# Kernel tuning notes

Measured on AMD Instinct MI355X. Metric: run time of the kernel, lower is better.

The kernel has to match this reference:

```python
import jax, jax.numpy as jnp
import numpy as np

B, S, HID = 2, 2048, 2048
NH, NKV, D = 32, 8, 64
G = NH // NKV  # kv groups


def rotate_half(x):
    x1, x2 = jnp.split(x, 2, axis=-1)
    return jnp.concatenate([-x2, x1], axis=-1)


def setup_inputs() -> dict:
    key = jax.random.key(0)
    ks = jax.random.split(key, 6)
    hidden_states = jax.random.normal(ks[0], (B, S, HID), dtype=jnp.float32)
    # rotary tables [S, D]
    inv_freq = 1.0 / (10000.0 ** (jnp.arange(0, D, 2, dtype=jnp.float32) / D))
    t = jnp.arange(S, dtype=jnp.float32)
    freqs = jnp.einsum('s,d->sd', t, inv_freq)
    emb = jnp.concatenate([freqs, freqs], axis=-1)
    cos, sin = jnp.cos(emb), jnp.sin(emb)
    # additive causal mask [B,1,S,S]
    causal = jnp.triu(jnp.full((S, S), -1e9, dtype=jnp.float32), k=1)
    attention_mask = jnp.broadcast_to(causal, (B, 1, S, S))
    sc = 0.02
    wq = jax.random.normal(ks[1], (HID, 2 * NH * D), dtype=jnp.float32) * sc
    wk = jax.random.normal(ks[2], (HID, NKV * D), dtype=jnp.float32) * sc
    wv = jax.random.normal(ks[3], (HID, NKV * D), dtype=jnp.float32) * sc
    wo = jax.random.normal(ks[4], (HID, HID), dtype=jnp.float32) * sc
    return {"hidden_states": hidden_states, "cos": cos, "sin": sin,
            "attention_mask": attention_mask, "wq": wq, "wk": wk, "wv": wv, "wo": wo}


def reference(hidden_states, cos, sin, attention_mask, wq, wk, wv, wo):
    b, s, _ = hidden_states.shape
    qg = hidden_states @ wq                      # [B,S,2*NH*D]
    q, gate = jnp.split(qg, 2, axis=-1)
    q = q.reshape(b, s, NH, D).transpose(0, 2, 1, 3)        # [B,NH,S,D]
    k = (hidden_states @ wk).reshape(b, s, NKV, D).transpose(0, 2, 1, 3)
    v = (hidden_states @ wv).reshape(b, s, NKV, D).transpose(0, 2, 1, 3)  # computed, unused (as in source)
    # RoPE (cos/sin broadcast over batch and heads)
    c = cos[None, None]; sn = sin[None, None]
    q = q * c + rotate_half(q) * sn
    k = k * c + rotate_half(k) * sn
    # GQA repeat_kv
    k = jnp.repeat(k, G, axis=1)                 # [B,NH,S,D]
    # no 1/sqrt(d) scaling in source
    attn = jnp.einsum('bhqd,bhkd->bhqk', q, k) + attention_mask
    w = jax.nn.softmax(attn.astype(jnp.float32), axis=-1).astype(q.dtype)
    # NOTE: source multiplies weights by key_states (not value_states) — reproduced faithfully
    out = jnp.einsum('bhqk,bhkd->bhqd', w, k)
    out = out.transpose(0, 2, 1, 3).reshape(b, s, HID)
    out = out * jax.nn.sigmoid(gate)
    return out @ wo
```

## Files before the change

kernel.cpp:

```cpp
#include <hip/hip_runtime.h>

typedef float f32x4 __attribute__((ext_vector_type(4)));
typedef short bf16x8 __attribute__((ext_vector_type(8)));

__device__ __forceinline__ float bf2f(unsigned short h) {
  return __uint_as_float(((unsigned int)h) << 16);
}
__device__ __forceinline__ unsigned short f2bf(float f) {
  unsigned int u = __float_as_uint(f);
  unsigned int r = u + 0x7fffu + ((u >> 16) & 1u);
  return (unsigned short)(r >> 16);
}
__device__ __forceinline__ float fast_exp2(float x) {
  return __builtin_amdgcn_exp2f(x);
}
__device__ __forceinline__ unsigned cvt_pk_bf16(float lo, float hi) {
  unsigned d;
  asm("v_cvt_pk_bf16_f32 %0, %1, %2" : "=v"(d) : "v"(lo), "v"(hi));
  return d;
}
__device__ __forceinline__ float max3f(float a, float b, float c) {
  float d;
  asm("v_max3_f32 %0, %1, %2, %3" : "=v"(d) : "v"(a), "v"(b), "v"(c));
  return d;
}

__device__ __forceinline__ void gload_lds16(const void* g, void* l) {
  __builtin_amdgcn_global_load_lds((const __attribute__((address_space(1))) void*)g,
                                   (__attribute__((address_space(3))) void*)l, 16, 0, 0);
}

__global__ void conv_bf16(const float* __restrict__ src, unsigned short* __restrict__ dst, int n4) {
  for (int i = blockIdx.x * blockDim.x + threadIdx.x; i < n4; i += gridDim.x * blockDim.x) {
    float4 v = ((const float4*)src)[i];
    ushort4 o;
    o.x = f2bf(v.x); o.y = f2bf(v.y); o.z = f2bf(v.z); o.w = f2bf(v.w);
    ((ushort4*)dst)[i] = o;
  }
}

__global__ void conv_cs(const float* __restrict__ cosT, const float* __restrict__ sinT,
                        unsigned* __restrict__ cs, int n) {
  int i = blockIdx.x * blockDim.x + threadIdx.x;
  if (i < n) cs[i] = cvt_pk_bf16(cosT[i], sinT[i]);
}

__global__ void tconv(const float* __restrict__ src, unsigned short* __restrict__ dst,
                      int C, int dstRowOff, int dstLD) {
  __shared__ float tile[32][33];
  int c0 = blockIdx.x * 32, r0 = blockIdx.y * 32;
  int tx = threadIdx.x, ty = threadIdx.y;
#pragma unroll
  for (int i = 0; i < 4; ++i)
    tile[ty + i * 8][tx] = src[(size_t)(r0 + ty + i * 8) * C + c0 + tx];
  __syncthreads();
#pragma unroll
  for (int i = 0; i < 4; ++i)
    dst[(size_t)(dstRowOff + c0 + ty + i * 8) * dstLD + r0 + tx] = f2bf(tile[tx][ty + i * 8]);
}

template <typename OutT>
__global__ __launch_bounds__(256) void gemm_bt(const unsigned short* __restrict__ A,
                                               const unsigned short* __restrict__ BT,
                                               OutT* __restrict__ C, int M, int N, int K) {
  __shared__ unsigned short As[128 * 64];
  __shared__ unsigned short Bs[128 * 64];
  const int tid = threadIdx.x;
  const int lane = tid & 63;
  const int wid = tid >> 6;
  const int g = lane >> 4, l15 = lane & 15;
  const int wr = wid >> 1, wc = wid & 1;
  const int bm = blockIdx.y, bn = blockIdx.x;
  const unsigned short* Ab = A + (size_t)bm * 128 * K;
  const unsigned short* Bb = BT + (size_t)bn * 128 * K;
  f32x4 acc[4][4] = {};
  int Rj[4], csj[4];
#pragma unroll
  for (int j = 0; j < 4; ++j) {
    int c = j * 256 + tid;
    Rj[j] = c >> 3;
    csj[j] = ((c & 7) ^ (Rj[j] & 7)) * 8;
  }
  for (int k0 = 0; k0 < K; k0 += 64) {
#pragma unroll
    for (int j = 0; j < 4; ++j) {
      gload_lds16(Ab + (size_t)Rj[j] * K + k0 + csj[j], &As[(j * 256 + (wid << 6)) * 8]);
      gload_lds16(Bb + (size_t)Rj[j] * K + k0 + csj[j], &Bs[(j * 256 + (wid << 6)) * 8]);
    }
    __syncthreads();
    bf16x8 af[4][2], bfr[4][2];
#pragma unroll
    for (int i = 0; i < 4; ++i)
#pragma unroll
      for (int kk = 0; kk < 2; ++kk) {
        int rowa = wr * 64 + i * 16 + l15;
        int cha = ((kk * 4 + g) ^ (rowa & 7)) * 8;
        af[i][kk] = *(const bf16x8*)&As[rowa * 64 + cha];
        int rowb = wc * 64 + i * 16 + l15;
        int chb = ((kk * 4 + g) ^ (rowb & 7)) * 8;
        bfr[i][kk] = *(const bf16x8*)&Bs[rowb * 64 + chb];
      }
    __builtin_amdgcn_s_setprio(1);
#pragma unroll
    for (int kk = 0; kk < 2; ++kk)
#pragma unroll
      for (int i = 0; i < 4; ++i)
#pragma unroll
        for (int j = 0; j < 4; ++j)
          acc[i][j] = __builtin_amdgcn_mfma_f32_16x16x32_bf16(af[i][kk], bfr[j][kk], acc[i][j], 0, 0, 0);
    __builtin_amdgcn_s_setprio(0);
    __syncthreads();
  }
  const int rbase = bm * 128 + wr * 64 + ((lane >> 4) << 2);
  const int cbase = bn * 128 + wc * 64 + l15;
#pragma unroll
  for (int i = 0; i < 4; ++i)
#pragma unroll
    for (int j = 0; j < 4; ++j)
#pragma unroll
      for (int r = 0; r < 4; ++r) {
        int row = rbase + i * 16 + r;
        int col = cbase + j * 16;
        if constexpr (sizeof(OutT) == 2)
          C[(size_t)row * N + col] = f2bf(acc[i][j][r]);
        else
          C[(size_t)row * N + col] = acc[i][j][r];
      }
}

__global__ __launch_bounds__(256) void gemm_qgk(const unsigned short* __restrict__ A,
                                                const unsigned short* __restrict__ BT,
                                                const unsigned* __restrict__ cs,
                                                unsigned short* __restrict__ qrope,
                                                unsigned short* __restrict__ gateb,
                                                unsigned short* __restrict__ krope) {
  const int K = 2048;
  __shared__ unsigned short As[128 * 64];
  __shared__ unsigned short Bs[128 * 64];
  const int tid = threadIdx.x;
  const int lane = tid & 63;
  const int wid = tid >> 6;
  const int g = lane >> 4, l15 = lane & 15;
  const int wr = wid >> 1, wc = wid & 1;
  const int bm = blockIdx.y, bn = blockIdx.x;
  const unsigned short* Ab = A + (size_t)bm * 128 * K;
  const unsigned short* Bb = BT + (size_t)bn * 128 * K;
  f32x4 acc[4][4] = {};
  int Rj[4], csj[4];
#pragma unroll
  for (int j = 0; j < 4; ++j) {
    int c = j * 256 + tid;
    Rj[j] = c >> 3;
    csj[j] = ((c & 7) ^ (Rj[j] & 7)) * 8;
  }
  for (int k0 = 0; k0 < K; k0 += 64) {
#pragma unroll
    for (int j = 0; j < 4; ++j) {
      gload_lds16(Ab + (size_t)Rj[j] * K + k0 + csj[j], &As[(j * 256 + (wid << 6)) * 8]);
      gload_lds16(Bb + (size_t)Rj[j] * K + k0 + csj[j], &Bs[(j * 256 + (wid << 6)) * 8]);
    }
    __syncthreads();
    bf16x8 af[4][2], bfr[4][2];
#pragma unroll
    for (int i = 0; i < 4; ++i)
#pragma unroll
      for (int kk = 0; kk < 2; ++kk) {
        int rowa = wr * 64 + i * 16 + l15;
        int cha = ((kk * 4 + g) ^ (rowa & 7)) * 8;
        af[i][kk] = *(const bf16x8*)&As[rowa * 64 + cha];
        int rowb = wc * 64 + i * 16 + l15;
        int chb = ((kk * 4 + g) ^ (rowb & 7)) * 8;
        bfr[i][kk] = *(const bf16x8*)&Bs[rowb * 64 + chb];
      }
    __builtin_amdgcn_s_setprio(1);
#pragma unroll
    for (int kk = 0; kk < 2; ++kk)
#pragma unroll
      for (int i = 0; i < 4; ++i)
#pragma unroll
        for (int j = 0; j < 4; ++j)
          acc[i][j] = __builtin_amdgcn_mfma_f32_16x16x32_bf16(af[i][kk], bfr[j][kk], acc[i][j], 0, 0, 0);
    __builtin_amdgcn_s_setprio(0);
    __syncthreads();
  }
  const int rbase = bm * 128 + wr * 64 + ((lane >> 4) << 2);
  if (bn < 16) {
    const int h = bn * 2 + wc;
#pragma unroll
    for (int i = 0; i < 4; ++i)
#pragma unroll
      for (int j = 0; j < 4; ++j)
#pragma unroll
        for (int r = 0; r < 4; ++r) {
          int row = rbase + i * 16 + r;
          int b = row >> 11, s = row & 2047;
          int d = j * 16 + l15;
          unsigned csv = cs[s * 64 + d];
          float c = bf2f((unsigned short)(csv & 0xffffu));
          float sn = bf2f((unsigned short)(csv >> 16));
          float x = acc[i][j][r], xp = acc[i][j ^ 2][r];
          float v = x * c + (((j & 2) == 0) ? -xp : xp) * sn;
          qrope[((size_t)(b * 32 + h) * 2048 + s) * 64 + d] = f2bf(v * 1.44269504089f);
        }
  } else if (bn < 32) {
    const int cb = (bn - 16) * 128 + wc * 64;
#pragma unroll
    for (int i = 0; i < 4; ++i)
#pragma unroll
      for (int j = 0; j < 4; ++j)
#pragma unroll
        for (int r = 0; r < 4; ++r) {
          int row = rbase + i * 16 + r;
          int b = row >> 11, s = row & 2047;
          gateb[(size_t)(b * 2048 + s) * 2048 + cb + j * 16 + l15] = f2bf(acc[i][j][r]);
        }
  } else {
    const int kh = (bn - 32) * 2 + wc;
#pragma unroll
    for (int i = 0; i < 4; ++i)
#pragma unroll
      for (int j = 0; j < 4; ++j)
#pragma unroll
        for (int r = 0; r < 4; ++r) {
          int row = rbase + i * 16 + r;
          int b = row >> 11, s = row & 2047;
          int d = j * 16 + l15;
          unsigned csv = cs[s * 64 + d];
          float c = bf2f((unsigned short)(csv & 0xffffu));
          float sn = bf2f((unsigned short)(csv >> 16));
          float x = acc[i][j][r], xp = acc[i][j ^ 2][r];
          float v = x * c + (((j & 2) == 0) ? -xp : xp) * sn;
          krope[((size_t)(b * 8 + kh) * 2048 + s) * 64 + d] = f2bf(v);
        }
  }
}

__global__ void ktrans(const unsigned short* __restrict__ krope, unsigned short* __restrict__ kT) {
  __shared__ unsigned short tile[64][65];
  int bh = blockIdx.y;
  int s0 = blockIdx.x * 64;
  const unsigned short* src = krope + (size_t)bh * 2048 * 64;
  unsigned short* dst = kT + (size_t)bh * 64 * 2048;
  int tx = threadIdx.x & 63, ty = threadIdx.x >> 6;
#pragma unroll
  for (int i = 0; i < 16; ++i)
    tile[ty + i * 4][tx] = src[(size_t)(s0 + ty + i * 4) * 64 + tx];
  __syncthreads();
#pragma unroll
  for (int i = 0; i < 16; ++i)
    dst[(size_t)(ty + i * 4) * 2048 + s0 + tx] = tile[tx][ty + i * 4];
}

__global__ __launch_bounds__(256) void attn_fused(const unsigned short* __restrict__ qrope,
                                                  const unsigned short* __restrict__ krope,
                                                  const unsigned short* __restrict__ kT,
                                                  const unsigned short* __restrict__ gateb,
                                                  unsigned short* __restrict__ attng) {
  __shared__ unsigned short Ks[2][64 * 64];
  __shared__ unsigned short KTs[2][64 * 64];
  __shared__ unsigned short Ps[128 * 64];
  const int qblk = 15 - blockIdx.y;
  const int bh = blockIdx.x;
  const int b = bh >> 5, h = bh & 31, kh = h >> 2;
  const int q0 = qblk * 128;
  const int tid = threadIdx.x, lane = tid & 63, wid = tid >> 6;
  const int g = lane >> 4, l15 = lane & 15;
  const unsigned short* Qbase = qrope + ((size_t)(b * 32 + h) * 2048 + q0) * 64;
  const unsigned short* Kbase = krope + (size_t)(b * 8 + kh) * 2048 * 64;
  const unsigned short* KTbase = kT + (size_t)(b * 8 + kh) * 64 * 2048;

#pragma unroll
  for (int j = 0; j < 4; ++j) {
    int F = ((j * 4 + wid) << 10) + (lane << 4);
    int R = F >> 7;
    int cs = ((F >> 4) & 7) ^ (R & 7);
    gload_lds16(Qbase + (size_t)R * 64 + cs * 8, &Ps[(j * 4 + wid) << 9]);
  }
  {
#pragma unroll
    for (int j = 0; j < 2; ++j) {
      int F = ((j * 4 + wid) << 10) + (lane << 4);
      int R = F >> 7;
      int cs = ((F >> 4) & 7) ^ (R & 7);
      gload_lds16(Kbase + (size_t)R * 64 + cs * 8, &Ks[0][(j * 4 + wid) << 9]);
      gload_lds16(KTbase + (size_t)R * 2048 + cs * 8, &KTs[0][(j * 4 + wid) << 9]);
    }
  }
  __syncthreads();

  bf16x8 qf[2][2];
#pragma unroll
  for (int i = 0; i < 2; ++i)
#pragma unroll
    for (int ks = 0; ks < 2; ++ks) {
      int row = wid * 32 + i * 16 + l15;
      int ch = (ks * 4 + g) ^ (row & 7);
      qf[i][ks] = *(const bf16x8*)&Ps[row * 64 + ch * 8];
    }
  __syncthreads();

  f32x4 oaccT[2][4] = {};
  float mrow[2] = {-1e30f, -1e30f}, lrow[2] = {0.f, 0.f};

  const int nt = 2 * qblk + 2;
  for (int t = 0; t < nt; ++t) {
    const int cur = t & 1;
    if (t + 1 < nt) {
      const int nb = cur ^ 1;
#pragma unroll
      for (int j = 0; j < 2; ++j) {
        int F = ((j * 4 + wid) << 10) + (lane << 4);
        int R = F >> 7;
        int cs = ((F >> 4) & 7) ^ (R & 7);
        gload_lds16(Kbase + (size_t)((t + 1) * 64 + R) * 64 + cs * 8, &Ks[nb][(j * 4 + wid) << 9]);
        gload_lds16(KTbase + (size_t)R * 2048 + (t + 1) * 64 + cs * 8, &KTs[nb][(j * 4 + wid) << 9]);
      }
    }
    f32x4 st[2][4] = {};
#pragma unroll
    for (int ks = 0; ks < 2; ++ks) {
      bf16x8 kf[4];
#pragma unroll
      for (int nf = 0; nf < 4; ++nf) {
        int row = nf * 16 + l15;
        int ch = (ks * 4 + g) ^ (row & 7);
        kf[nf] = *(const bf16x8*)&Ks[cur][row * 64 + ch * 8];
      }
      __builtin_amdgcn_s_setprio(1);
#pragma unroll
      for (int i = 0; i < 2; ++i)
#pragma unroll
        for (int nf = 0; nf < 4; ++nf)
          st[i][nf] = __builtin_amdgcn_mfma_f32_16x16x32_bf16(kf[nf], qf[i][ks], st[i][nf], 0, 0, 0);
      __builtin_amdgcn_s_setprio(0);
    }
    if (t >= 2 * qblk) {
#pragma unroll
      for (int i = 0; i < 2; ++i) {
        int qabs = q0 + wid * 32 + i * 16 + l15;
#pragma unroll
        for (int nf = 0; nf < 4; ++nf)
#pragma unroll
          for (int r = 0; r < 4; ++r) {
            int kabs = t * 64 + nf * 16 + 4 * g + r;
            if (kabs > qabs) st[i][nf][r] += -1e9f;
          }
      }
    }
#pragma unroll
    for (int i = 0; i < 2; ++i) {
      float a0 = max3f(st[i][0][0], st[i][0][1], st[i][0][2]);
      float a1 = max3f(st[i][0][3], st[i][1][0], st[i][1][1]);
      float a2 = max3f(st[i][1][2], st[i][1][3], st[i][2][0]);
      float a3 = max3f(st[i][2][1], st[i][2][2], st[i][2][3]);
      float a4 = max3f(st[i][3][0], st[i][3][1], st[i][3][2]);
      float pm = fmaxf(max3f(a0, a1, a2), max3f(a3, a4, st[i][3][3]));
      pm = fmaxf(pm, __shfl_xor(pm, 16, 64));
      pm = fmaxf(pm, __shfl_xor(pm, 32, 64));
      if (!__all(pm <= mrow[i] + 8.f)) {
        float mnew = fmaxf(mrow[i], pm);
        float scale = fast_exp2(mrow[i] - mnew);
        mrow[i] = mnew;
        lrow[i] *= scale;
#pragma unroll
        for (int df = 0; df < 4; ++df)
#pragma unroll
          for (int r = 0; r < 4; ++r) oaccT[i][df][r] *= scale;
      }
      float rs = 0.f;
#pragma unroll
      for (int nf = 0; nf < 4; ++nf)
#pragma unroll
        for (int r = 0; r < 4; ++r) {
          float p = fast_exp2(st[i][nf][r] - mrow[i]);
          st[i][nf][r] = p;
          rs += p;
        }
      rs += __shfl_xor(rs, 16, 64);
      rs += __shfl_xor(rs, 32, 64);
      lrow[i] += rs;
    }
#pragma unroll
    for (int i = 0; i < 2; ++i) {
      int q = wid * 32 + i * 16 + l15;
#pragma unroll
      for (int nf = 0; nf < 4; ++nf) {
        int k0 = nf * 16 + 4 * g;
        int ch = (k0 >> 3) ^ (q & 7);
        unsigned w0 = cvt_pk_bf16(st[i][nf][0], st[i][nf][1]);
        unsigned w1 = cvt_pk_bf16(st[i][nf][2], st[i][nf][3]);
        *(uint2*)&Ps[q * 64 + ch * 8 + (k0 & 7)] = make_uint2(w0, w1);
      }
    }
#pragma unroll
    for (int ks = 0; ks < 2; ++ks) {
      bf16x8 pf[2], vf[4];
#pragma unroll
      for (int i = 0; i < 2; ++i) {
        int row = wid * 32 + i * 16 + l15;
        int ch = (ks * 4 + g) ^ (row & 7);
        pf[i] = *(const bf16x8*)&Ps[row * 64 + ch * 8];
      }
#pragma unroll
      for (int df = 0; df < 4; ++df) {
        int row = df * 16 + l15;
        int ch = (ks * 4 + g) ^ (row & 7);
        vf[df] = *(const bf16x8*)&KTs[cur][row * 64 + ch * 8];
      }
      __builtin_amdgcn_s_setprio(1);
#pragma unroll
      for (int i = 0; i < 2; ++i)
#pragma unroll
        for (int df = 0; df < 4; ++df)
          oaccT[i][df] = __builtin_amdgcn_mfma_f32_16x16x32_bf16(vf[df], pf[i], oaccT[i][df], 0, 0, 0);
      __builtin_amdgcn_s_setprio(0);
    }
    __syncthreads();
  }
#pragma unroll
  for (int i = 0; i < 2; ++i) {
    float rl = 1.f / lrow[i];
    int qabs = q0 + wid * 32 + i * 16 + l15;
    size_t grow = (size_t)b * 2048 + qabs;
#pragma unroll
    for (int df = 0; df < 4; ++df) {
      int d0 = df * 16 + 4 * g;
      ushort4 gt = *(const ushort4*)&gateb[grow * 2048 + h * 64 + d0];
      float o0 = oaccT[i][df][0] * rl * (1.f / (1.f + __expf(-bf2f(gt.x))));
      float o1 = oaccT[i][df][1] * rl * (1.f / (1.f + __expf(-bf2f(gt.y))));
      float o2 = oaccT[i][df][2] * rl * (1.f / (1.f + __expf(-bf2f(gt.z))));
      float o3 = oaccT[i][df][3] * rl * (1.f / (1.f + __expf(-bf2f(gt.w))));
      *(uint2*)&attng[grow * 2048 + h * 64 + d0] =
          make_uint2(cvt_pk_bf16(o0, o1), cvt_pk_bf16(o2, o3));
    }
  }
}

extern "C" void kernel_launch(void* const* d_in, const int* in_sizes, int n_in,
                              void* d_out, int out_size, void* d_ws, size_t ws_size,
                              hipStream_t stream) {
  const float* hidden = (const float*)d_in[0];
  const float* cosT = (const float*)d_in[1];
  const float* sinT = (const float*)d_in[2];
  const float* wq = (const float*)d_in[4];
  const float* wk = (const float*)d_in[5];
  const float* wo = (const float*)d_in[7];
  char* ws = (char*)d_ws;
  unsigned short* hb16  = (unsigned short*)(ws + 0);
  unsigned short* wcatT = (unsigned short*)(ws + 16777216);
  unsigned short* woT   = (unsigned short*)(ws + 35651584);
  unsigned short* gateb = (unsigned short*)(ws + 44040192);
  unsigned short* qrope = (unsigned short*)(ws + 60817408);
  unsigned short* krope = (unsigned short*)(ws + 77594624);
  unsigned short* kTb   = (unsigned short*)(ws + 81788928);
  unsigned short* attng = (unsigned short*)(ws + 85983232);
  unsigned*       csT   = (unsigned*)(ws + 102760448);

  conv_bf16<<<dim3(2048), dim3(256), 0, stream>>>(hidden, hb16, 2097152);
  conv_cs<<<dim3(512), dim3(256), 0, stream>>>(cosT, sinT, csT, 131072);
  tconv<<<dim3(128, 64), dim3(32, 8), 0, stream>>>(wq, wcatT, 4096, 0, 2048);
  tconv<<<dim3(16, 64), dim3(32, 8), 0, stream>>>(wk, wcatT, 512, 4096, 2048);
  tconv<<<dim3(64, 64), dim3(32, 8), 0, stream>>>(wo, woT, 2048, 0, 2048);
  gemm_qgk<<<dim3(36, 32), dim3(256), 0, stream>>>(hb16, wcatT, csT,
                                                   qrope, gateb, krope);
  ktrans<<<dim3(32, 16), dim3(256), 0, stream>>>(krope, kTb);
  attn_fused<<<dim3(64, 16), dim3(256), 0, stream>>>(qrope, krope, kTb, gateb, attng);
  gemm_bt<float><<<dim3(16, 32), dim3(256), 0, stream>>>(attng, woT, (float*)d_out, 4096, 2048, 2048);
}
```

Measured before the change: 252.2 us.

## Enlarge attention key tile from 64 to 128 keys per iteration

The fused attention kernel now processes 128 keys per loop iteration instead of 64, which halves the number of iterations, barriers and softmax max/rescale passes per query block. K and K-transposed shared-memory buffers are doubled, and the transposed tile uses a 16-way swizzle. The P tile is written and consumed in two 64-key halves so the P buffer keeps its size. In exchange, shared memory rises to about 80KB per block, which may reduce occupancy, registers grow with the doubled score array, and the diagonal tile now masks more work.

```diff
diff --git a/kernel.cpp b/kernel.cpp
--- a/kernel.cpp
+++ b/kernel.cpp
@@ -256,8 +256,8 @@
                                                   const unsigned short* __restrict__ kT,
                                                   const unsigned short* __restrict__ gateb,
                                                   unsigned short* __restrict__ attng) {
-  __shared__ unsigned short Ks[2][64 * 64];
-  __shared__ unsigned short KTs[2][64 * 64];
+  __shared__ unsigned short Ks[2][128 * 64];
+  __shared__ unsigned short KTs[2][64 * 128];
   __shared__ unsigned short Ps[128 * 64];
   const int qblk = 15 - blockIdx.y;
   const int bh = blockIdx.x;
@@ -273,18 +273,22 @@
   for (int j = 0; j < 4; ++j) {
     int F = ((j * 4 + wid) << 10) + (lane << 4);
     int R = F >> 7;
-    int cs = ((F >> 4) & 7) ^ (R & 7);
-    gload_lds16(Qbase + (size_t)R * 64 + cs * 8, &Ps[(j * 4 + wid) << 9]);
-  }
-  {
-#pragma unroll
-    for (int j = 0; j < 2; ++j) {
-      int F = ((j * 4 + wid) << 10) + (lane << 4);
-      int R = F >> 7;
-      int cs = ((F >> 4) & 7) ^ (R & 7);
-      gload_lds16(Kbase + (size_t)R * 64 + cs * 8, &Ks[0][(j * 4 + wid) << 9]);
-      gload_lds16(KTbase + (size_t)R * 2048 + cs * 8, &KTs[0][(j * 4 + wid) << 9]);
-    }
+    int csw = ((F >> 4) & 7) ^ (R & 7);
+    gload_lds16(Qbase + (size_t)R * 64 + csw * 8, &Ps[(j * 4 + wid) << 9]);
+  }
+#pragma unroll
+  for (int j = 0; j < 4; ++j) {
+    int F = ((j * 4 + wid) << 10) + (lane << 4);
+    int R = F >> 7;
+    int csw = ((F >> 4) & 7) ^ (R & 7);
+    gload_lds16(Kbase + (size_t)R * 64 + csw * 8, &Ks[0][(j * 4 + wid) << 9]);
+  }
+#pragma unroll
+  for (int j = 0; j < 4; ++j) {
+    int c = j * 256 + tid;
+    int R = c >> 4;
+    int csw = (c & 15) ^ (R & 15);
+    gload_lds16(KTbase + (size_t)R * 2048 + csw * 8, &KTs[0][c * 8]);
   }
   __syncthreads();
 
@@ -302,59 +306,68 @@
   f32x4 oaccT[2][4] = {};
   float mrow[2] = {-1e30f, -1e30f}, lrow[2] = {0.f, 0.f};
 
-  const int nt = 2 * qblk + 2;
+  const int nt = qblk + 1;
   for (int t = 0; t < nt; ++t) {
     const int cur = t & 1;
     if (t + 1 < nt) {
       const int nb = cur ^ 1;
 #pragma unroll
-      for (int j = 0; j < 2; ++j) {
+      for (int j = 0; j < 4; ++j) {
         int F = ((j * 4 + wid) << 10) + (lane << 4);
         int R = F >> 7;
-        int cs = ((F >> 4) & 7) ^ (R & 7);
-        gload_lds16(Kbase + (size_t)((t + 1) * 64 + R) * 64 + cs * 8, &Ks[nb][(j * 4 + wid) << 9]);
-        gload_lds16(KTbase + (size_t)R * 2048 + (t + 1) * 64 + cs * 8, &KTs[nb][(j * 4 + wid) << 9]);
-      }
-    }
-    f32x4 st[2][4] = {};
-#pragma unroll
-    for (int ks = 0; ks < 2; ++ks) {
-      bf16x8 kf[4];
-#pragma unroll
-      for (int nf = 0; nf < 4; ++nf) {
-        int row = nf * 16 + l15;
-        int ch = (ks * 4 + g) ^ (row & 7);
-        kf[nf] = *(const bf16x8*)&Ks[cur][row * 64 + ch * 8];
-      }
-      __builtin_amdgcn_s_setprio(1);
-#pragma unroll
-      for (int i = 0; i < 2; ++i)
-#pragma unroll
-        for (int nf = 0; nf < 4; ++nf)
-          st[i][nf] = __builtin_amdgcn_mfma_f32_16x16x32_bf16(kf[nf], qf[i][ks], st[i][nf], 0, 0, 0);
-      __builtin_amdgcn_s_setprio(0);
-    }
-    if (t >= 2 * qblk) {
+        int csw = ((F >> 4) & 7) ^ (R & 7);
+        gload_lds16(Kbase + (size_t)((t + 1) * 128 + R) * 64 + csw * 8, &Ks[nb][(j * 4 + wid) << 9]);
+      }
+#pragma unroll
+      for (int j = 0; j < 4; ++j) {
+        int c = j * 256 + tid;
+        int R = c >> 4;
+        int csw = (c & 15) ^ (R & 15);
+        gload_lds16(KTbase + (size_t)R * 2048 + (t + 1) * 128 + csw * 8, &KTs[nb][c * 8]);
+      }
+    }
+    f32x4 st[2][8] = {};
+#pragma unroll
+    for (int ks = 0; ks < 2; ++ks)
+#pragma unroll
+      for (int nq = 0; nq < 2; ++nq) {
+        bf16x8 kf[4];
+#pragma unroll
+        for (int f = 0; f < 4; ++f) {
+          int row = (nq * 4 + f) * 16 + l15;
+          int ch = (ks * 4 + g) ^ (row & 7);
+          kf[f] = *(const bf16x8*)&Ks[cur][row * 64 + ch * 8];
+        }
+        __builtin_amdgcn_s_setprio(1);
+#pragma unroll
+        for (int i = 0; i < 2; ++i)
+#pragma unroll
+          for (int f = 0; f < 4; ++f)
+            st[i][nq * 4 + f] =
+                __builtin_amdgcn_mfma_f32_16x16x32_bf16(kf[f], qf[i][ks], st[i][nq * 4 + f], 0, 0, 0);
+        __builtin_amdgcn_s_setprio(0);
+      }
+    if (t == nt - 1) {
 #pragma unroll
       for (int i = 0; i < 2; ++i) {
         int qabs = q0 + wid * 32 + i * 16 + l15;
 #pragma unroll
-        for (int nf = 0; nf < 4; ++nf)
+        for (int nf = 0; nf < 8; ++nf)
 #pragma unroll
           for (int r = 0; r < 4; ++r) {
-            int kabs = t * 64 + nf * 16 + 4 * g + r;
+            int kabs = t * 128 + nf * 16 + 4 * g + r;
             if (kabs > qabs) st[i][nf][r] += -1e9f;
           }
       }
     }
 #pragma unroll
     for (int i = 0; i < 2; ++i) {
-      float a0 = max3f(st[i][0][0], st[i][0][1], st[i][0][2]);
-      float a1 = max3f(st[i][0][3], st[i][1][0], st[i][1][1]);
-      float a2 = max3f(st[i][1][2], st[i][1][3], st[i][2][0]);
-      float a3 = max3f(st[i][2][1], st[i][2][2], st[i][2][3]);
-      float a4 = max3f(st[i][3][0], st[i][3][1], st[i][3][2]);
-      float pm = fmaxf(max3f(a0, a1, a2), max3f(a3, a4, st[i][3][3]));
+      float pm = -1e30f;
+#pragma unroll
+      for (int nf = 0; nf < 8; ++nf) {
+        pm = max3f(pm, st[i][nf][0], st[i][nf][1]);
+        pm = max3f(pm, st[i][nf][2], st[i][nf][3]);
+      }
       pm = fmaxf(pm, __shfl_xor(pm, 16, 64));
       pm = fmaxf(pm, __shfl_xor(pm, 32, 64));
       if (!__all(pm <= mrow[i] + 8.f)) {
@@ -369,7 +382,7 @@
       }
       float rs = 0.f;
 #pragma unroll
-      for (int nf = 0; nf < 4; ++nf)
+      for (int nf = 0; nf < 8; ++nf)
 #pragma unroll
         for (int r = 0; r < 4; ++r) {
           float p = fast_exp2(st[i][nf][r] - mrow[i]);
@@ -381,39 +394,44 @@
       lrow[i] += rs;
     }
 #pragma unroll
-    for (int i = 0; i < 2; ++i) {
-      int q = wid * 32 + i * 16 + l15;
-#pragma unroll
-      for (int nf = 0; nf < 4; ++nf) {
-        int k0 = nf * 16 + 4 * g;
-        int ch = (k0 >> 3) ^ (q & 7);
-        unsigned w0 = cvt_pk_bf16(st[i][nf][0], st[i][nf][1]);
-        unsigned w1 = cvt_pk_bf16(st[i][nf][2], st[i][nf][3]);
-        *(uint2*)&Ps[q * 64 + ch * 8 + (k0 & 7)] = make_uint2(w0, w1);
-      }
-    }
-#pragma unroll
-    for (int ks = 0; ks < 2; ++ks) {
-      bf16x8 pf[2], vf[4];
+    for (int half = 0; half < 2; ++half) {
 #pragma unroll
       for (int i = 0; i < 2; ++i) {
-        int row = wid * 32 + i * 16 + l15;
-        int ch = (ks * 4 + g) ^ (row & 7);
-        pf[i] = *(const bf16x8*)&Ps[row * 64 + ch * 8];
-      }
-#pragma unroll
-      for (int df = 0; df < 4; ++df) {
-        int row = df * 16 + l15;
-        int ch = (ks * 4 + g) ^ (row & 7);
-        vf[df] = *(const bf16x8*)&KTs[cur][row * 64 + ch * 8];
-      }
-      __builtin_amdgcn_s_setprio(1);
-#pragma unroll
-      for (int i = 0; i < 2; ++i)
-#pragma unroll
-        for (int df = 0; df < 4; ++df)
-          oaccT[i][df] = __builtin_amdgcn_mfma_f32_16x16x32_bf16(vf[df], pf[i], oaccT[i][df], 0, 0, 0);
-      __builtin_amdgcn_s_setprio(0);
+        int q = wid * 32 + i * 16 + l15;
+#pragma unroll
+        for (int f = 0; f < 4; ++f) {
+          int nf = half * 4 + f;
+          int k0 = f * 16 + 4 * g;
+          int ch = (k0 >> 3) ^ (q & 7);
+          unsigned w0 = cvt_pk_bf16(st[i][nf][0], st[i][nf][1]);
+          unsigned w1 = cvt_pk_bf16(st[i][nf][2], st[i][nf][3]);
+          *(uint2*)&Ps[q * 64 + ch * 8 + (k0 & 7)] = make_uint2(w0, w1);
+        }
+      }
+#pragma unroll
+      for (int ks2 = 0; ks2 < 2; ++ks2) {
+        const int ksg = half * 2 + ks2;
+        bf16x8 pf[2], vf[4];
+#pragma unroll
+        for (int i = 0; i < 2; ++i) {
+          int row = wid * 32 + i * 16 + l15;
+          int ch = (ks2 * 4 + g) ^ (row & 7);
+          pf[i] = *(const bf16x8*)&Ps[row * 64 + ch * 8];
+        }
+#pragma unroll
+        for (int df = 0; df < 4; ++df) {
+          int row = df * 16 + l15;
+          int ch = (ksg * 4 + g) ^ (row & 15);
+          vf[df] = *(const bf16x8*)&KTs[cur][row * 128 + ch * 8];
+        }
+        __builtin_amdgcn_s_setprio(1);
+#pragma unroll
+        for (int i = 0; i < 2; ++i)
+#pragma unroll
+          for (int df = 0; df < 4; ++df)
+            oaccT[i][df] = __builtin_amdgcn_mfma_f32_16x16x32_bf16(vf[df], pf[i], oaccT[i][df], 0, 0, 0);
+        __builtin_amdgcn_s_setprio(0);
+      }
     }
     __syncthreads();
   }
```

Result: slower. 269.7 us (+7.0%).
